# Kernel optimization log

Measured on AMD Instinct MI355X. Metric: run time of the kernel, lower is better.

The kernel has to match this reference:

```python
import jax, jax.numpy as jnp
import numpy as np

NUM_HEADS = 16
NEG_INF = -1e30


def setup_inputs() -> dict:
    key = jax.random.key(0)
    k1, k2, k3 = jax.random.split(key, 3)
    B, S, D = 2, 2048, 1024
    x = jax.random.normal(k1, (B, S, D), dtype=jnp.float32)
    # torch Linear(D, 3D, bias=False) stored here already transposed: y = x @ w_qkv
    w_qkv = jax.random.normal(k2, (D, 3 * D), dtype=jnp.float32) * 0.02
    w_out = jax.random.normal(k3, (D, D), dtype=jnp.float32) * 0.02
    return {"x": x, "w_qkv": w_qkv, "w_out": w_out}


def reference(x, w_qkv, w_out):
    B, S, D = x.shape
    H = NUM_HEADS
    dh = D // H
    qkv = x @ w_qkv                      # [B, S, 3D]
    q, k, v = jnp.split(qkv, 3, axis=-1)

    def to_heads(t):
        return t.reshape(B, S, H, dh).transpose(0, 2, 1, 3)  # [B, H, S, dh]

    q, k, v = to_heads(q), to_heads(k), to_heads(v)
    scale = jnp.asarray(dh, x.dtype) ** -0.5
    scores = jnp.einsum('bhqd,bhkd->bhqk', q, k) * scale     # [B, H, S, S]
    causal = jnp.tril(jnp.ones((S, S), dtype=bool))
    scores = jnp.where(causal, scores, NEG_INF)
    attn = jax.nn.softmax(scores, axis=-1)
    out = jnp.einsum('bhqk,bhkd->bhqd', attn, v)             # [B, H, S, dh]
    out = out.transpose(0, 2, 1, 3).reshape(B, S, D)
    return out @ w_out
```

## Files before the change

kernel.cpp:

```cpp
#include <hip/hip_runtime.h>

typedef unsigned short u16;
typedef unsigned int u32;

typedef __bf16 bf16x8 __attribute__((ext_vector_type(8)));
typedef _Float16 f16x8 __attribute__((ext_vector_type(8)));
typedef float f32x4 __attribute__((ext_vector_type(4)));

typedef __attribute__((address_space(1))) u32 as1_u32;
typedef __attribute__((address_space(3))) u32 as3_u32;

#define EKF 0.18033688011112042f

__device__ __forceinline__ u16 f2bf(float x) {
  u32 u = __float_as_uint(x);
  u = u + 0x7fffu + ((u >> 16) & 1u);
  return (u16)(u >> 16);
}
__device__ __forceinline__ u32 pack2(float a, float b) {
  return (u32)f2bf(a) | ((u32)f2bf(b) << 16);
}
__device__ __forceinline__ u32 pkf16(float a, float b) {
  return __builtin_bit_cast(u32, __builtin_amdgcn_cvt_pkrtz(a, b));
}
__device__ __forceinline__ u16 f2h(float a) {
  return (u16)(pkf16(a, a) & 0xffffu);
}
__device__ __forceinline__ void gld_lds16(const u16* g, const u16* l) {
  __builtin_amdgcn_global_load_lds((const as1_u32*)g, (as3_u32*)l, 16, 0, 0);
}

__global__ void cvt_bf16_kernel(const float* __restrict__ in, u16* __restrict__ out, int n4) {
  int i = blockIdx.x * blockDim.x + threadIdx.x;
  if (i < n4) {
    float4 v = ((const float4*)in)[i];
    uint2 r;
    r.x = pack2(v.x, v.y);
    r.y = pack2(v.z, v.w);
    ((uint2*)out)[i] = r;
  }
}

__global__ __launch_bounds__(256) void transpose_bf16_tiled(const float* __restrict__ W,
                                                            u16* __restrict__ WT,
                                                            int K, int N) {
  __shared__ float tile[64][65];
  int k0 = blockIdx.x * 64, n0 = blockIdx.y * 64;
  int t = threadIdx.x;
  int r = t >> 4, c4 = (t & 15) * 4;
#pragma unroll
  for (int i = 0; i < 4; ++i) {
    int row = r + i * 16;
    float4 v = *(const float4*)&W[(size_t)(k0 + row) * N + n0 + c4];
    tile[row][c4 + 0] = v.x; tile[row][c4 + 1] = v.y;
    tile[row][c4 + 2] = v.z; tile[row][c4 + 3] = v.w;
  }
  __syncthreads();
#pragma unroll
  for (int i = 0; i < 4; ++i) {
    int n = r + i * 16;
    uint2 o;
    o.x = pack2(tile[c4 + 0][n], tile[c4 + 1][n]);
    o.y = pack2(tile[c4 + 2][n], tile[c4 + 3][n]);
    *(uint2*)&WT[(size_t)(n0 + n) * K + k0 + c4] = o;
  }
}

__global__ __launch_bounds__(256) void transpose_vt_kernel(const u16* __restrict__ vtmp,
                                                           u16* __restrict__ vt) {
  __shared__ u16 t[64 * 71];
  int j0 = blockIdx.x * 64;
  int bh = blockIdx.y;
  int b = bh >> 4, h = bh & 15;
  int tid = threadIdx.x;
  int r = tid >> 2, cs = (tid & 3) * 16;
  const u16* src = vtmp + (size_t)(b * 2048 + j0 + r) * 1024 + h * 64 + cs;
  uint4 a = ((const uint4*)src)[0];
  uint4 c = ((const uint4*)src)[1];
  u16* dst = &t[r * 71 + cs];
  dst[0] = (u16)a.x; dst[1] = (u16)(a.x >> 16); dst[2] = (u16)a.y; dst[3] = (u16)(a.y >> 16);
  dst[4] = (u16)a.z; dst[5] = (u16)(a.z >> 16); dst[6] = (u16)a.w; dst[7] = (u16)(a.w >> 16);
  dst[8] = (u16)c.x; dst[9] = (u16)(c.x >> 16); dst[10] = (u16)c.y; dst[11] = (u16)(c.y >> 16);
  dst[12] = (u16)c.z; dst[13] = (u16)(c.z >> 16); dst[14] = (u16)c.w; dst[15] = (u16)(c.w >> 16);
  __syncthreads();
  int d = tid >> 2, jseg = (tid & 3) * 16;
  u32 w[8];
#pragma unroll
  for (int i = 0; i < 8; ++i) {
    u32 lo = t[(jseg + 2 * i) * 71 + d];
    u32 hi = t[(jseg + 2 * i + 1) * 71 + d];
    w[i] = lo | (hi << 16);
  }
  u16* out = vt + (size_t)(bh * 64 + d) * 2048 + j0 + jseg;
  ((uint4*)out)[0] = make_uint4(w[0], w[1], w[2], w[3]);
  ((uint4*)out)[1] = make_uint4(w[4], w[5], w[6], w[7]);
}

template <int OUT_MODE, int BN>
__global__ __launch_bounds__(256) void gemm_bt_kernel(const u16* __restrict__ A,
                                                      const u16* __restrict__ BT,
                                                      void* __restrict__ Cv,
                                                      u16* __restrict__ VT,
                                                      int M, int N, int K) {
  const int NF = (BN == 128) ? 4 : 2;
  __shared__ __attribute__((aligned(16))) u16 sA[128 * 32];
  __shared__ __attribute__((aligned(16))) u16 sB[BN * 32];
  const int tid = threadIdx.x;
  const int wave = tid >> 6;
  const int lane = tid & 63;
  const int bm = blockIdx.y * 128;
  const int bn = blockIdx.x * BN;
  const int wm = (wave >> 1) * 64;
  const int wn = (wave & 1) * (BN / 2);
  const int lr = lane & 15;
  const int kg = lane >> 4;

  const int srow = tid >> 2;
  const int scol = (tid & 3) * 8;
  const u16* pa0 = A + (size_t)(bm + srow) * K + scol;
  const u16* pa1 = pa0 + (size_t)64 * K;
  const u16* pb0 = BT + (size_t)(bn + srow) * K + scol;
  const u16* pb1 = pb0 + (size_t)64 * K;
  const u16* la = sA + wave * 512;
  const u16* lb = sB + wave * 512;

  f32x4 acc[4][NF];
#pragma unroll
  for (int i = 0; i < 4; i++)
#pragma unroll
    for (int j = 0; j < NF; j++) {
      f32x4 z = {0.f, 0.f, 0.f, 0.f};
      acc[i][j] = z;
    }

  for (int k0 = 0; k0 < K; k0 += 32) {
    __syncthreads();
    gld_lds16(pa0 + k0, la);
    gld_lds16(pa1 + k0, la + 2048);
    gld_lds16(pb0 + k0, lb);
    if (BN == 128) gld_lds16(pb1 + k0, lb + 2048);
    __syncthreads();
    bf16x8 af[4], bfr[NF];
#pragma unroll
    for (int mi = 0; mi < 4; mi++)
      af[mi] = *(const bf16x8*)(sA + (wm + mi * 16 + lr) * 32 + kg * 8);
#pragma unroll
    for (int ni = 0; ni < NF; ni++)
      bfr[ni] = *(const bf16x8*)(sB + (wn + ni * 16 + lr) * 32 + kg * 8);
#pragma unroll
    for (int mi = 0; mi < 4; mi++)
#pragma unroll
      for (int ni = 0; ni < NF; ni++)
        acc[mi][ni] = __builtin_amdgcn_mfma_f32_16x16x32_bf16(af[mi], bfr[ni], acc[mi][ni], 0, 0, 0);
  }

#pragma unroll
  for (int mi = 0; mi < 4; mi++)
#pragma unroll
    for (int ni = 0; ni < NF; ni++) {
      int c = bn + wn + ni * 16 + lr;
      int r0 = bm + wm + mi * 16 + kg * 4;
      if (OUT_MODE == 0) {
#pragma unroll
        for (int rr = 0; rr < 4; rr++)
          ((float*)Cv)[(size_t)(r0 + rr) * N + c] = acc[mi][ni][rr];
      } else {
        if (c < 1024) {
          u16* qkp = (u16*)Cv;
#pragma unroll
          for (int rr = 0; rr < 4; rr++)
            qkp[(size_t)(r0 + rr) * 2048 + c] = f2bf(acc[mi][ni][rr] * EKF);
        } else if (c < 2048) {
          u16* qkp = (u16*)Cv;
#pragma unroll
          for (int rr = 0; rr < 4; rr++)
            qkp[(size_t)(r0 + rr) * 2048 + c] = f2bf(acc[mi][ni][rr]);
        } else {
          int cc = c - 2048;
#pragma unroll
          for (int rr = 0; rr < 4; rr++)
            VT[(size_t)(r0 + rr) * 1024 + cc] = f2h(acc[mi][ni][rr]);
        }
      }
    }
}

__global__ __launch_bounds__(256) void attn_mfma_kernel(const u16* __restrict__ qk,
                                                        const u16* __restrict__ vt,
                                                        u16* __restrict__ out) {
  __shared__ __attribute__((aligned(16))) u16 sQ[2][64 * 32];
  __shared__ __attribute__((aligned(16))) u16 sK[2][128 * 32];
  __shared__ __attribute__((aligned(16))) u16 sV[4][64 * 32];
  __shared__ __attribute__((aligned(16))) u16 sP[4][16 * 72];

  const int tid = threadIdx.x;
  const int wave = tid >> 6;
  const int lane = tid & 63;
  const int lq = lane & 15;
  const int lg = lane >> 4;

  int idx = blockIdx.x;
  int qc = 31 - (idx >> 5);
  int bh = idx & 31;
  int b = bh >> 4, h = bh & 15;
  int q0 = qc * 64;

  const u16* qbase = qk + (size_t)b * 2048 * 2048 + h * 64;
  const u16* kbase = qbase + 1024;
  const u16* vbase = vt + (size_t)bh * 64 * 2048;
  u16* obase = out + (size_t)b * 2048 * 1024 + h * 64;

#pragma unroll
  for (int it = 0; it < 2; ++it) {
    int rows0 = ((wave & 1) * 2 + it) * 16;
    int row = rows0 + (lane >> 2);
    gld_lds16(qbase + (size_t)(q0 + row) * 2048 + (wave >> 1) * 32 + (lane & 3) * 8,
              sQ[wave >> 1] + rows0 * 32);
  }
  __syncthreads();

  bf16x8 qf0 = *(const bf16x8*)(sQ[0] + (wave * 16 + lq) * 32 + lg * 8);
  bf16x8 qf1 = *(const bf16x8*)(sQ[1] + (wave * 16 + lq) * 32 + lg * 8);

  float lsum = 0.f;
  f32x4 oacc[4];
#pragma unroll
  for (int i = 0; i < 4; ++i) {
    f32x4 z = {0.f, 0.f, 0.f, 0.f};
    oacc[i] = z;
  }

  u16* const pw = sP[wave] + lq * 72 + lg * 4;
  const u16* const pr = sP[wave] + lq * 72 + lg * 8;
  const int wqmax = q0 + wave * 16 + 15;

  const int rounds = (qc + 2) >> 1;
  for (int r = 0; r < rounds; ++r) {
    int j0 = r * 128;
    __syncthreads();
#pragma unroll
    for (int it = 0; it < 4; ++it) {
      int rows0 = ((wave & 1) * 4 + it) * 16;
      int row = rows0 + (lane >> 2);
      gld_lds16(kbase + (size_t)(j0 + row) * 2048 + (wave >> 1) * 32 + (lane & 3) * 8,
                sK[wave >> 1] + rows0 * 32);
    }
#pragma unroll
    for (int it = 0; it < 4; ++it) {
      int rows0 = it * 16;
      int drow = rows0 + (lane >> 2);
      gld_lds16(vbase + (size_t)drow * 2048 + j0 + wave * 32 + (lane & 3) * 8,
                sV[wave] + rows0 * 32);
    }
    __syncthreads();

#pragma unroll
    for (int u = 0; u < 2; ++u) {
      int js = j0 + u * 64;
      if (js > wqmax) continue;
      const u16* sKu = sK[0] + u * 64 * 32;
      const u16* sKu1 = sK[1] + u * 64 * 32;

      if (js < q0) {
#pragma unroll
        for (int jt = 0; jt < 4; ++jt) {
          bf16x8 kf0 = *(const bf16x8*)(sKu + (jt * 16 + lq) * 32 + lg * 8);
          bf16x8 kf1 = *(const bf16x8*)(sKu1 + (jt * 16 + lq) * 32 + lg * 8);
          f32x4 c = {0.f, 0.f, 0.f, 0.f};
          c = __builtin_amdgcn_mfma_f32_16x16x32_bf16(kf0, qf0, c, 0, 0, 0);
          c = __builtin_amdgcn_mfma_f32_16x16x32_bf16(kf1, qf1, c, 0, 0, 0);
          float p0 = exp2f(c[0]);
          float p1 = exp2f(c[1]);
          float p2 = exp2f(c[2]);
          float p3 = exp2f(c[3]);
          lsum += (p0 + p1) + (p2 + p3);
          *(uint2*)(pw + jt * 16) = make_uint2(pkf16(p0, p1), pkf16(p2, p3));
        }
      } else {
#pragma unroll
        for (int jt = 0; jt < 4; ++jt) {
          if (jt <= wave) {
            bf16x8 kf0 = *(const bf16x8*)(sKu + (jt * 16 + lq) * 32 + lg * 8);
            bf16x8 kf1 = *(const bf16x8*)(sKu1 + (jt * 16 + lq) * 32 + lg * 8);
            f32x4 c = {0.f, 0.f, 0.f, 0.f};
            c = __builtin_amdgcn_mfma_f32_16x16x32_bf16(kf0, qf0, c, 0, 0, 0);
            c = __builtin_amdgcn_mfma_f32_16x16x32_bf16(kf1, qf1, c, 0, 0, 0);
            float p0 = exp2f(c[0]);
            float p1 = exp2f(c[1]);
            float p2 = exp2f(c[2]);
            float p3 = exp2f(c[3]);
            if (jt == wave) {
              int jr = lg * 4;
              p0 = (jr + 0 <= lq) ? p0 : 0.f;
              p1 = (jr + 1 <= lq) ? p1 : 0.f;
              p2 = (jr + 2 <= lq) ? p2 : 0.f;
              p3 = (jr + 3 <= lq) ? p3 : 0.f;
            }
            lsum += (p0 + p1) + (p2 + p3);
            *(uint2*)(pw + jt * 16) = make_uint2(pkf16(p0, p1), pkf16(p2, p3));
          } else {
            *(uint2*)(pw + jt * 16) = make_uint2(0u, 0u);
          }
        }
      }

      asm volatile("" ::: "memory");

      f16x8 pf0 = *(const f16x8*)(pr);
      f16x8 pf1 = *(const f16x8*)(pr + 32);
      const u16* sVu = sV[u * 2];
      const u16* sVu1 = sV[u * 2 + 1];
#pragma unroll
      for (int dt = 0; dt < 4; ++dt) {
        f16x8 vf0 = *(const f16x8*)(sVu + (dt * 16 + lq) * 32 + lg * 8);
        f16x8 vf1 = *(const f16x8*)(sVu1 + (dt * 16 + lq) * 32 + lg * 8);
        oacc[dt] = __builtin_amdgcn_mfma_f32_16x16x32_f16(vf0, pf0, oacc[dt], 0, 0, 0);
        oacc[dt] = __builtin_amdgcn_mfma_f32_16x16x32_f16(vf1, pf1, oacc[dt], 0, 0, 0);
      }
    }
  }

  lsum += __shfl_xor(lsum, 16);
  lsum += __shfl_xor(lsum, 32);
  float inv = 1.0f / lsum;

#pragma unroll
  for (int dt = 0; dt < 4; ++dt) {
    int d = dt * 16 + lg * 4;
    u32 lo = pack2(oacc[dt][0] * inv, oacc[dt][1] * inv);
    u32 hi = pack2(oacc[dt][2] * inv, oacc[dt][3] * inv);
    *(uint2*)(obase + (size_t)(q0 + wave * 16 + lq) * 1024 + d) = make_uint2(lo, hi);
  }
}

extern "C" void kernel_launch(void* const* d_in, const int* in_sizes, int n_in,
                              void* d_out, int out_size, void* d_ws, size_t ws_size,
                              hipStream_t stream) {
  const float* x = (const float*)d_in[0];
  const float* w_qkv = (const float*)d_in[1];
  const float* w_out = (const float*)d_in[2];
  float* out = (float*)d_out;

  char* ws = (char*)d_ws;
  u16* xb    = (u16*)(ws);
  u16* wqkvT = (u16*)(ws + (8u << 20));
  u16* woutT = (u16*)(ws + (14u << 20));
  u16* qkb   = (u16*)(ws + (16u << 20));
  u16* vtb   = (u16*)(ws + (32u << 20));
  u16* vtmp  = (u16*)(ws + (40u << 20));
  u16* attn  = (u16*)(ws + (40u << 20));

  cvt_bf16_kernel<<<4096, 256, 0, stream>>>(x, xb, 4194304 / 4);
  transpose_bf16_tiled<<<dim3(16, 48), 256, 0, stream>>>(w_qkv, wqkvT, 1024, 3072);
  transpose_bf16_tiled<<<dim3(16, 16), 256, 0, stream>>>(w_out, woutT, 1024, 1024);

  gemm_bt_kernel<2, 128><<<dim3(3072 / 128, 4096 / 128), 256, 0, stream>>>(
      xb, wqkvT, (void*)qkb, vtmp, 4096, 3072, 1024);

  transpose_vt_kernel<<<dim3(32, 32), 256, 0, stream>>>(vtmp, vtb);

  attn_mfma_kernel<<<1024, 256, 0, stream>>>(qkb, vtb, attn);

  gemm_bt_kernel<0, 64><<<dim3(1024 / 64, 4096 / 128), 256, 0, stream>>>(
      attn, woutT, (void*)out, nullptr, 4096, 1024, 1024);
}
```

Before: 194.2 us.

## Rewrite attention kernel with 32x32 MFMA tiles and 128-row query blocks

```diff
diff --git a/kernel.cpp b/kernel.cpp
--- a/kernel.cpp
+++ b/kernel.cpp
@@ -6,6 +6,7 @@
 typedef __bf16 bf16x8 __attribute__((ext_vector_type(8)));
 typedef _Float16 f16x8 __attribute__((ext_vector_type(8)));
 typedef float f32x4 __attribute__((ext_vector_type(4)));
+typedef float f32x16 __attribute__((ext_vector_type(16)));
 
 typedef __attribute__((address_space(1))) u32 as1_u32;
 typedef __attribute__((address_space(3))) u32 as3_u32;
@@ -185,152 +186,140 @@
     }
 }
 
-__global__ __launch_bounds__(256) void attn_mfma_kernel(const u16* __restrict__ qk,
-                                                        const u16* __restrict__ vt,
-                                                        u16* __restrict__ out) {
-  __shared__ __attribute__((aligned(16))) u16 sQ[2][64 * 32];
-  __shared__ __attribute__((aligned(16))) u16 sK[2][128 * 32];
-  __shared__ __attribute__((aligned(16))) u16 sV[4][64 * 32];
-  __shared__ __attribute__((aligned(16))) u16 sP[4][16 * 72];
+__global__ __launch_bounds__(256, 3) void attn_mfma_kernel(const u16* __restrict__ qk,
+                                                           const u16* __restrict__ vt,
+                                                           u16* __restrict__ out) {
+  __shared__ __attribute__((aligned(16))) u16 sK[64 * 64];
+  __shared__ __attribute__((aligned(16))) u16 sV[64 * 64];
+  __shared__ __attribute__((aligned(16))) u16 sP[4][32 * 48];
 
   const int tid = threadIdx.x;
   const int wave = tid >> 6;
   const int lane = tid & 63;
-  const int lq = lane & 15;
-  const int lg = lane >> 4;
+  const int lq = lane & 31;
+  const int g = lane >> 5;
+  const int l7 = lane & 7;
 
   int idx = blockIdx.x;
-  int qc = 31 - (idx >> 5);
+  int qi = 15 - (idx >> 5);
   int bh = idx & 31;
   int b = bh >> 4, h = bh & 15;
-  int q0 = qc * 64;
+  int q0 = qi * 128;
 
   const u16* qbase = qk + (size_t)b * 2048 * 2048 + h * 64;
   const u16* kbase = qbase + 1024;
   const u16* vbase = vt + (size_t)bh * 64 * 2048;
   u16* obase = out + (size_t)b * 2048 * 1024 + h * 64;
 
-#pragma unroll
-  for (int it = 0; it < 2; ++it) {
-    int rows0 = ((wave & 1) * 2 + it) * 16;
-    int row = rows0 + (lane >> 2);
-    gld_lds16(qbase + (size_t)(q0 + row) * 2048 + (wave >> 1) * 32 + (lane & 3) * 8,
-              sQ[wave >> 1] + rows0 * 32);
-  }
-  __syncthreads();
-
-  bf16x8 qf0 = *(const bf16x8*)(sQ[0] + (wave * 16 + lq) * 32 + lg * 8);
-  bf16x8 qf1 = *(const bf16x8*)(sQ[1] + (wave * 16 + lq) * 32 + lg * 8);
-
+  const int qcol = q0 + wave * 32 + lq;
+  bf16x8 qf[4];
+  {
+    const u16* qrow = qbase + (size_t)qcol * 2048;
+#pragma unroll
+    for (int ks = 0; ks < 4; ++ks)
+      qf[ks] = *(const bf16x8*)(qrow + ks * 16 + g * 8);
+  }
+
+  bool dmask[16];
+#pragma unroll
+  for (int a = 0; a < 16; ++a)
+    dmask[a] = ((a & 3) + 8 * (a >> 2) + 4 * g) <= lq;
+
+  f32x16 oacc[2];
+#pragma unroll
+  for (int i = 0; i < 16; ++i) { oacc[0][i] = 0.f; oacc[1][i] = 0.f; }
   float lsum = 0.f;
-  f32x4 oacc[4];
-#pragma unroll
-  for (int i = 0; i < 4; ++i) {
-    f32x4 z = {0.f, 0.f, 0.f, 0.f};
-    oacc[i] = z;
-  }
-
-  u16* const pw = sP[wave] + lq * 72 + lg * 4;
-  const u16* const pr = sP[wave] + lq * 72 + lg * 8;
-  const int wqmax = q0 + wave * 16 + 15;
-
-  const int rounds = (qc + 2) >> 1;
-  for (int r = 0; r < rounds; ++r) {
-    int j0 = r * 128;
+
+  const int sr = tid >> 2;
+  const int se = (tid & 3) * 16;
+  const int sc0 = (tid & 3) * 2;
+  const int sr7 = sr & 7;
+  u16* const skw0 = sK + sr * 64 + ((sc0 ^ sr7) * 8);
+  u16* const skw1 = sK + sr * 64 + (((sc0 + 1) ^ sr7) * 8);
+  u16* const svw0 = sV + sr * 64 + ((sc0 ^ sr7) * 8);
+  u16* const svw1 = sV + sr * 64 + (((sc0 + 1) ^ sr7) * 8);
+
+  u16* const sPw = sP[wave];
+  const int smax = wave + 4 * qi;
+
+  const int nrounds = 2 * qi + 2;
+  for (int t = 0; t < nrounds; ++t) {
+    int j0 = t * 64;
     __syncthreads();
-#pragma unroll
-    for (int it = 0; it < 4; ++it) {
-      int rows0 = ((wave & 1) * 4 + it) * 16;
-      int row = rows0 + (lane >> 2);
-      gld_lds16(kbase + (size_t)(j0 + row) * 2048 + (wave >> 1) * 32 + (lane & 3) * 8,
-                sK[wave >> 1] + rows0 * 32);
-    }
-#pragma unroll
-    for (int it = 0; it < 4; ++it) {
-      int rows0 = it * 16;
-      int drow = rows0 + (lane >> 2);
-      gld_lds16(vbase + (size_t)drow * 2048 + j0 + wave * 32 + (lane & 3) * 8,
-                sV[wave] + rows0 * 32);
+    {
+      const u16* kg_ = kbase + (size_t)(j0 + sr) * 2048 + se;
+      uint4 ka = ((const uint4*)kg_)[0];
+      uint4 kb = ((const uint4*)kg_)[1];
+      const u16* vg = vbase + (size_t)sr * 2048 + j0 + se;
+      uint4 va = ((const uint4*)vg)[0];
+      uint4 vb = ((const uint4*)vg)[1];
+      *(uint4*)skw0 = ka;
+      *(uint4*)skw1 = kb;
+      *(uint4*)svw0 = va;
+      *(uint4*)svw1 = vb;
     }
     __syncthreads();
 
 #pragma unroll
-    for (int u = 0; u < 2; ++u) {
-      int js = j0 + u * 64;
-      if (js > wqmax) continue;
-      const u16* sKu = sK[0] + u * 64 * 32;
-      const u16* sKu1 = sK[1] + u * 64 * 32;
-
-      if (js < q0) {
-#pragma unroll
-        for (int jt = 0; jt < 4; ++jt) {
-          bf16x8 kf0 = *(const bf16x8*)(sKu + (jt * 16 + lq) * 32 + lg * 8);
-          bf16x8 kf1 = *(const bf16x8*)(sKu1 + (jt * 16 + lq) * 32 + lg * 8);
-          f32x4 c = {0.f, 0.f, 0.f, 0.f};
-          c = __builtin_amdgcn_mfma_f32_16x16x32_bf16(kf0, qf0, c, 0, 0, 0);
-          c = __builtin_amdgcn_mfma_f32_16x16x32_bf16(kf1, qf1, c, 0, 0, 0);
-          float p0 = exp2f(c[0]);
-          float p1 = exp2f(c[1]);
-          float p2 = exp2f(c[2]);
-          float p3 = exp2f(c[3]);
-          lsum += (p0 + p1) + (p2 + p3);
-          *(uint2*)(pw + jt * 16) = make_uint2(pkf16(p0, p1), pkf16(p2, p3));
-        }
+    for (int jt = 0; jt < 2; ++jt) {
+      int s = 2 * t + jt;
+      if (s > smax) continue;
+
+      f32x16 st;
+#pragma unroll
+      for (int i = 0; i < 16; ++i) st[i] = 0.f;
+#pragma unroll
+      for (int ks = 0; ks < 4; ++ks) {
+        bf16x8 kf = *(const bf16x8*)(sK + (jt * 32 + lq) * 64 + (((ks * 2 + g) ^ l7) * 8));
+        st = __builtin_amdgcn_mfma_f32_32x32x16_bf16(kf, qf[ks], st, 0, 0, 0);
+      }
+
+      float p[16];
+      if (s == smax) {
+#pragma unroll
+        for (int a = 0; a < 16; ++a) p[a] = dmask[a] ? exp2f(st[a]) : 0.f;
       } else {
 #pragma unroll
-        for (int jt = 0; jt < 4; ++jt) {
-          if (jt <= wave) {
-            bf16x8 kf0 = *(const bf16x8*)(sKu + (jt * 16 + lq) * 32 + lg * 8);
-            bf16x8 kf1 = *(const bf16x8*)(sKu1 + (jt * 16 + lq) * 32 + lg * 8);
-            f32x4 c = {0.f, 0.f, 0.f, 0.f};
-            c = __builtin_amdgcn_mfma_f32_16x16x32_bf16(kf0, qf0, c, 0, 0, 0);
-            c = __builtin_amdgcn_mfma_f32_16x16x32_bf16(kf1, qf1, c, 0, 0, 0);
-            float p0 = exp2f(c[0]);
-            float p1 = exp2f(c[1]);
-            float p2 = exp2f(c[2]);
-            float p3 = exp2f(c[3]);
-            if (jt == wave) {
-              int jr = lg * 4;
-              p0 = (jr + 0 <= lq) ? p0 : 0.f;
-              p1 = (jr + 1 <= lq) ? p1 : 0.f;
-              p2 = (jr + 2 <= lq) ? p2 : 0.f;
-              p3 = (jr + 3 <= lq) ? p3 : 0.f;
-            }
-            lsum += (p0 + p1) + (p2 + p3);
-            *(uint2*)(pw + jt * 16) = make_uint2(pkf16(p0, p1), pkf16(p2, p3));
-          } else {
-            *(uint2*)(pw + jt * 16) = make_uint2(0u, 0u);
-          }
+        for (int a = 0; a < 16; ++a) p[a] = exp2f(st[a]);
+      }
+#pragma unroll
+      for (int a = 0; a < 16; ++a) lsum += p[a];
+
+      u16* pwv = sPw + lq * 48 + g * 4;
+#pragma unroll
+      for (int tq = 0; tq < 4; ++tq)
+        *(uint2*)(pwv + tq * 8) =
+            make_uint2(pkf16(p[4 * tq + 0], p[4 * tq + 1]),
+                       pkf16(p[4 * tq + 2], p[4 * tq + 3]));
+
+      asm volatile("" ::: "memory");
+
+#pragma unroll
+      for (int ks = 0; ks < 2; ++ks) {
+        f16x8 pf = *(const f16x8*)(sPw + lq * 48 + ks * 16 + g * 8);
+#pragma unroll
+        for (int dt = 0; dt < 2; ++dt) {
+          f16x8 vf = *(const f16x8*)(sV + (dt * 32 + lq) * 64 +
+                                     (((jt * 4 + ks * 2 + g) ^ l7) * 8));
+          oacc[dt] = __builtin_amdgcn_mfma_f32_32x32x16_f16(vf, pf, oacc[dt], 0, 0, 0);
         }
       }
-
-      asm volatile("" ::: "memory");
-
-      f16x8 pf0 = *(const f16x8*)(pr);
-      f16x8 pf1 = *(const f16x8*)(pr + 32);
-      const u16* sVu = sV[u * 2];
-      const u16* sVu1 = sV[u * 2 + 1];
-#pragma unroll
-      for (int dt = 0; dt < 4; ++dt) {
-        f16x8 vf0 = *(const f16x8*)(sVu + (dt * 16 + lq) * 32 + lg * 8);
-        f16x8 vf1 = *(const f16x8*)(sVu1 + (dt * 16 + lq) * 32 + lg * 8);
-        oacc[dt] = __builtin_amdgcn_mfma_f32_16x16x32_f16(vf0, pf0, oacc[dt], 0, 0, 0);
-        oacc[dt] = __builtin_amdgcn_mfma_f32_16x16x32_f16(vf1, pf1, oacc[dt], 0, 0, 0);
-      }
-    }
-  }
-
-  lsum += __shfl_xor(lsum, 16);
+    }
+  }
+
   lsum += __shfl_xor(lsum, 32);
   float inv = 1.0f / lsum;
 
-#pragma unroll
-  for (int dt = 0; dt < 4; ++dt) {
-    int d = dt * 16 + lg * 4;
-    u32 lo = pack2(oacc[dt][0] * inv, oacc[dt][1] * inv);
-    u32 hi = pack2(oacc[dt][2] * inv, oacc[dt][3] * inv);
-    *(uint2*)(obase + (size_t)(q0 + wave * 16 + lq) * 1024 + d) = make_uint2(lo, hi);
-  }
+  u16* orow = obase + (size_t)qcol * 1024;
+#pragma unroll
+  for (int dt = 0; dt < 2; ++dt)
+#pragma unroll
+    for (int tq = 0; tq < 4; ++tq) {
+      int d = dt * 32 + 8 * tq + 4 * g;
+      uint2 o2 = make_uint2(pack2(oacc[dt][4 * tq + 0] * inv, oacc[dt][4 * tq + 1] * inv),
+                            pack2(oacc[dt][4 * tq + 2] * inv, oacc[dt][4 * tq + 3] * inv));
+      *(uint2*)(orow + d) = o2;
+    }
 }
 
 extern "C" void kernel_launch(void* const* d_in, const int* in_sizes, int n_in,
@@ -359,7 +348,7 @@
 
   transpose_vt_kernel<<<dim3(32, 32), 256, 0, stream>>>(vtmp, vtb);
 
-  attn_mfma_kernel<<<1024, 256, 0, stream>>>(qkb, vtb, attn);
+  attn_mfma_kernel<<<512, 256, 0, stream>>>(qkb, vtb, attn);
 
   gemm_bt_kernel<0, 64><<<dim3(1024 / 64, 4096 / 128), 256, 0, stream>>>(
       attn, woutT, (void*)out, nullptr, 4096, 1024, 1024);
```

Result: slower. 209.6 us (+7.9%).
